# Performance work log

Hardware: AMD Instinct MI355X
Metric: run time of the kernel (lower is better)

## Reference

```python
import jax, jax.numpy as jnp
import numpy as np

GAMMA = 0.3   # LinearSpike surrogate slope
THR = 1.0     # default_threshold (all layers)
LEAK = 1.0
T = 20        # timesteps

# ---- surrogate-gradient spike functions ----
@jax.custom_vjp
def lin_spike(u):
    # forward: heaviside(u > 0); backward: gamma * max(1-|u|, 0)
    return (u > 0.0).astype(u.dtype)

def _ls_fwd(u):
    return lin_spike(u), u

def _ls_bwd(u, g):
    return (GAMMA * jnp.maximum(1.0 - jnp.abs(u), 0.0) * g,)

lin_spike.defvjp(_ls_fwd, _ls_bwd)

@jax.custom_vjp
def rect_spike(v):
    # threshold_rect: heaviside(v > 1); backward: 1[|v-1| < 0.5]
    return (v > 1.0).astype(v.dtype)

def _rs_fwd(v):
    return rect_spike(v), v

def _rs_bwd(v, g):
    return ((jnp.abs(v - 1.0) < 0.5).astype(g.dtype) * g,)

rect_spike.defvjp(_rs_fwd, _rs_bwd)


def conv3(x, w):
    # 3x3 conv, stride 1, SAME padding, no bias (matches bias=False Conv2d)
    return jax.lax.conv_general_dilated(
        x, w, (1, 1), 'SAME', dimension_numbers=('NCHW', 'OIHW', 'NCHW'))


def pool2(x):
    # AvgPool2d(kernel=2, stride=2)
    b, c, h, w = x.shape
    return x.reshape(b, c, h // 2, 2, w // 2, 2).mean(axis=(3, 5))


def setup_inputs() -> dict:
    key = jax.random.key(0)
    ks = jax.random.split(key, 7)
    B = 16
    x = jax.random.uniform(ks[0], (B, 3, 32, 32), jnp.float32)  # image in [0,1]

    def he(k, shape):  # _initialize_weights2 for conv: N(0, sqrt(2/(k*k*out_ch)))
        n = shape[0] * shape[2] * shape[3]
        return jax.random.normal(k, shape, jnp.float32) * np.float32(np.sqrt(2.0 / n))

    W1 = he(ks[1], (64, 3, 3, 3))
    W2 = he(ks[2], (128, 64, 3, 3))
    W3 = he(ks[3], (128, 128, 3, 3))
    # linears: N(0, 0.01), bias=False
    L1 = jax.random.normal(ks[4], (1024, 8192), jnp.float32) * 0.01
    L2 = jax.random.normal(ks[5], (1024, 1024), jnp.float32) * 0.01
    L3 = jax.random.normal(ks[6], (10, 1024), jnp.float32) * 0.01
    return {"x": x, "W1": W1, "W2": W2, "W3": W3, "L1": L1, "L2": L2, "L3": L3}


def reference(x, W1, W2, W3, L1, L2, L3):
    B = x.shape[0]
    dt = x.dtype
    z = lambda s: jnp.zeros(s, dt)
    carry = (z(x.shape), z(x.shape),           # encoder membrane v, last spike
             z((B, 64, 32, 32)),               # mem conv1
             z((B, 128, 16, 16)),              # mem conv2
             z((B, 128, 16, 16)),              # mem conv3
             z((B, 1024)), z((B, 1024)),       # mem fc1, fc2
             z((B, 10)))                       # output membrane (accumulator)

    def lif(mem, inp):
        # spike from current mem, soft reset by threshold, leaky integrate input
        out = lin_spike(mem / THR - 1.0)
        return LEAK * mem + inp - THR * out, out

    def step(c, _):
        v, s, m1, m2, m3, m4, m5, mo = c
        # if_encoder forward_2, soft reset: v = v + x*max_rate - spike
        v = v + x - s
        s = rect_spike(v)
        m1, o1 = lif(m1, conv3(s, W1))
        o1 = pool2(o1)                         # 32 -> 16
        m2, o2 = lif(m2, conv3(o1, W2))
        m3, o3 = lif(m3, conv3(o2, W3))
        f = pool2(o3).reshape(B, -1)           # 16 -> 8; flatten to 8192
        m4, o4 = lif(m4, f @ L1.T)
        m5, o5 = lif(m5, o4 @ L2.T)
        mo = mo + o5 @ L3.T                    # final linear accumulates membrane
        return (v, s, m1, m2, m3, m4, m5, mo), None

    carry, _ = jax.lax.scan(step, carry, None, length=T)
    return carry[-1]
```

## Files before the change

kernel.cpp:

```cpp
#include <hip/hip_runtime.h>

constexpr int BB   = 16;
constexpr int VS   = BB*3*32*32;
constexpr int M1N  = BB*64*32*32;
constexpr int O1PN = BB*64*18*20;
constexpr int M2N  = BB*128*16*16;
constexpr int O2PN = BB*128*18*20;
constexpr int M3N  = M2N;
constexpr int FBN  = BB*8192;
constexpr int M4N  = BB*1024;
constexpr int M5N  = BB*1024;

constexpr int off_v   = 0;
constexpr int off_s   = off_v   + 2*VS;
constexpr int off_m1  = off_s   + 2*VS;
constexpr int off_o1p = off_m1  + M1N;
constexpr int off_m2  = off_o1p + 2*O1PN;
constexpr int off_o2p = off_m2  + M2N;
constexpr int off_m3  = off_o2p + 2*O2PN;
constexpr int off_f   = off_m3  + M3N;
constexpr int off_m4  = off_f   + 2*FBN;
constexpr int off_o4  = off_m4  + M4N;
constexpr int off_m5  = off_o4  + 2*M4N;
constexpr int off_o5  = off_m5  + M5N;
constexpr int off_w1r = off_o5  + 2*M5N;
constexpr int W1RN = 64*3*12;
constexpr int off_w2r = off_w1r + W1RN;
constexpr int W2RN = 8*8*64*20;
constexpr int off_w3r = off_w2r + W2RN;
constexpr int W3RN = 8*8*128*20;
constexpr int TOTF = off_w3r + W3RN;

__device__ __forceinline__ float4 ld4(const float* p){ return *reinterpret_cast<const float4*>(p); }
__device__ __forceinline__ float2 ld2(const float* p){ return *reinterpret_cast<const float2*>(p); }
__device__ __forceinline__ float spk(float m){ return m > 1.0f ? 1.0f : 0.0f; }

__device__ __forceinline__ void gll16(const float* g, float* l) {
    __builtin_amdgcn_global_load_lds(
        (const __attribute__((address_space(1))) unsigned int*)g,
        (__attribute__((address_space(3))) unsigned int*)(unsigned int)(unsigned long long)l,
        16, 0, 0);
}

__global__ __launch_bounds__(256) void init_k(const float* __restrict__ W1,
                                              const float* __restrict__ W2,
                                              const float* __restrict__ W3,
                                              float* __restrict__ ws,
                                              float* __restrict__ out) {
    int i0 = blockIdx.x*256 + threadIdx.x;
    int stride = gridDim.x*256;
    for (int p = i0; p < TOTF; p += stride) {
        float val = 0.0f;
        if (p >= off_w1r) {
            if (p < off_w2r) {
                int l = p - off_w1r, q = l/12, r = l%12;
                int dx = r & 3, dy = r >> 2;
                val = (dx < 3) ? W1[q*9 + dy*3 + dx] : 0.0f;
            } else if (p < off_w3r) {
                int l = p - off_w2r;
                int cog = l / 10240, rem = l % 10240;
                int pr = rem / 1280, rem2 = rem % 1280;
                int ci = rem2 / 20, k = rem2 % 20;
                if (k < 18) {
                    int co = cog*16 + pr*2 + (k >= 9 ? 1 : 0);
                    int kk = k >= 9 ? k - 9 : k;
                    val = W2[(co*64 + ci)*9 + kk];
                }
            } else {
                int l = p - off_w3r;
                int cog = l / 20480, rem = l % 20480;
                int pr = rem / 2560, rem2 = rem % 2560;
                int ci = rem2 / 20, k = rem2 % 20;
                if (k < 18) {
                    int co = cog*16 + pr*2 + (k >= 9 ? 1 : 0);
                    int kk = k >= 9 ? k - 9 : k;
                    val = W3[(co*128 + ci)*9 + kk];
                }
            }
        }
        ws[p] = val;
    }
    if (i0 < 160) out[i0] = 0.0f;
}

#define CVW_LOAD(W, WQ) do {                                                   \
    _Pragma("unroll") for (int q_ = 0; q_ < 5; ++q_) W[q_] = ld4((WQ) + q_*4); } while(0)

#define CV4_FMA(Iu, Iv, W) do {                                                \
    float rv[4][6];                                                            \
    _Pragma("unroll") for (int r_ = 0; r_ < 4; ++r_) {                         \
        rv[r_][0]=Iu[r_].x; rv[r_][1]=Iu[r_].y; rv[r_][2]=Iu[r_].z;            \
        rv[r_][3]=Iu[r_].w; rv[r_][4]=Iv[r_].x; rv[r_][5]=Iv[r_].y; }          \
    float wd[2][9] = {{W[0].x,W[0].y,W[0].z,W[0].w,W[1].x,W[1].y,W[1].z,W[1].w,W[2].x}, \
                      {W[2].y,W[2].z,W[2].w,W[3].x,W[3].y,W[3].z,W[3].w,W[4].x,W[4].y}}; \
    _Pragma("unroll") for (int cc_ = 0; cc_ < 2; ++cc_)                        \
      _Pragma("unroll") for (int iy_ = 0; iy_ < 2; ++iy_)                      \
        _Pragma("unroll") for (int dy_ = 0; dy_ < 3; ++dy_)                    \
          _Pragma("unroll") for (int dx_ = 0; dx_ < 3; ++dx_) {                \
            float wv_ = wd[cc_][dy_*3+dx_];                                    \
            _Pragma("unroll") for (int p_ = 0; p_ < 4; ++p_)                   \
              acc[cc_][iy_][p_] += rv[iy_+dy_][p_+dx_]*wv_; } } while(0)

#define CVL_READ(Iu, Iv, P) do {                                               \
    _Pragma("unroll") for (int r_ = 0; r_ < 4; ++r_) {                         \
        Iu[r_] = ld4((P) + r_*28); Iv[r_] = ld2((P) + r_*28 + 4); } } while(0)

#define CV_STAGE(BUF, CH) do {                                                 \
    _Pragma("unroll") for (int k_ = 0; k_ < 4; ++k_) {                         \
        if (k_*256 + tid < 1008)                                               \
            gll16(gip + (CH)*2880 + ssrc[k_], sh + (BUF)*4032 + sdst[k_]);     \
    } } while(0)

__global__ __launch_bounds__(256) void step_k(const float* __restrict__ x,
                                              const float* __restrict__ L1,
                                              const float* __restrict__ L2,
                                              const float* __restrict__ L3,
                                              float* __restrict__ ws,
                                              float* __restrict__ out,
                                              int t) {
    const int rp = t & 1, wp = rp ^ 1;
    const int bid = blockIdx.x, tid = threadIdx.x;
    __shared__ __align__(16) float sh[8064];

    if (bid < 256) {
        const bool is3 = bid < 128;
        int bb = is3 ? bid : bid - 128;
        int b = bb >> 3, cog = bb & 7;
        int cl = tid >> 5, rest = tid & 31, rpair = rest >> 2, cg = rest & 3;
        int y0 = rpair*2, x0 = cg*4;
        int co = cog*16 + cl*2;
        const int NCI = is3 ? 128 : 64;
        const float* gip = is3 ? (ws + off_o2p + rp*O2PN + b*128*360)
                               : (ws + off_o1p + rp*O1PN + b*64*360);
        const float* wpt = is3 ? (ws + off_w3r + (cog*8 + cl)*128*20)
                               : (ws + off_w2r + (cog*8 + cl)*64*20);
        int ssrc[4], sdst[4];
        #pragma unroll
        for (int k = 0; k < 4; ++k) {
            int c = k*256 + tid;
            int u = c/126, rem = c - u*126, r = rem/7, j = rem - r*7;
            ssrc[k] = u*360 + (j < 5 ? 20*r + 4*j : 0);
            sdst[k] = c*4;
        }
        float acc[2][2][4] = {};
        float4 WA[5], WB[5];
        CVW_LOAD(WA, wpt);
        CVW_LOAD(WB, wpt + 20);
        CV_STAGE(0, 0);
        __syncthreads();
        const int NCH = NCI >> 3;
        #pragma unroll 1
        for (int ch = 0; ch < NCH; ++ch) {
            if (ch + 1 < NCH) CV_STAGE((ch+1)&1, ch+1);
            const float* lb = sh + (ch&1)*4032 + y0*28 + x0;
            #pragma unroll 1
            for (int u = 0; u < 8; u += 2) {
                int ci = ch*8 + u;
                {
                    float4 IAu[4]; float2 IAv[4];
                    CVL_READ(IAu, IAv, lb + u*504);
                    CV4_FMA(IAu, IAv, WA);
                    if (ci + 2 < NCI) CVW_LOAD(WA, wpt + (ci+2)*20);
                }
                {
                    float4 IBu[4]; float2 IBv[4];
                    CVL_READ(IBu, IBv, lb + u*504 + 504);
                    CV4_FMA(IBu, IBv, WB);
                    if (ci + 3 < NCI) CVW_LOAD(WB, wpt + (ci+3)*20);
                }
            }
            __syncthreads();
        }
        if (is3) {
            #pragma unroll
            for (int cc = 0; cc < 2; ++cc) {
                float sp[2][4];
                #pragma unroll
                for (int iy = 0; iy < 2; ++iy)
                    #pragma unroll
                    for (int p = 0; p < 4; ++p) {
                        int gm = off_m3 + ((b*128 + co + cc)*16 + y0 + iy)*16 + x0 + p;
                        float m = ws[gm], o = spk(m);
                        float mn = m + acc[cc][iy][p] - o;
                        ws[gm] = mn;
                        sp[iy][p] = spk(mn);
                    }
                int fbase = off_f + wp*FBN + b*8192 + (co + cc)*64 + (y0>>1)*8 + (x0>>1);
                ws[fbase+0] = (sp[0][0]+sp[0][1]+sp[1][0]+sp[1][1])*0.25f;
                ws[fbase+1] = (sp[0][2]+sp[0][3]+sp[1][2]+sp[1][3])*0.25f;
            }
        } else {
            #pragma unroll
            for (int cc = 0; cc < 2; ++cc) {
                #pragma unroll
                for (int iy = 0; iy < 2; ++iy) {
                    int mbase = off_m2 + ((b*128 + co + cc)*16 + y0 + iy)*16 + x0;
                    int obase = off_o2p + wp*O2PN + ((b*128 + co + cc)*18 + y0 + iy + 1)*20 + x0 + 1;
                    #pragma unroll
                    for (int p = 0; p < 4; ++p) {
                        float m = ws[mbase+p], o = spk(m);
                        float mn = m + acc[cc][iy][p] - o;
                        ws[mbase+p] = mn;
                        ws[obase+p] = spk(mn);
                    }
                }
            }
        }
    } else if (bid < 384) {
        int jb = bid - 256;
        int w = tid >> 6, l = tid & 63;
        const float* fp = ws + off_f + rp*FBN;
        const float* wb = L1 + (jb*8 + w*2)*8192;
        float acc[2][16] = {};
        float4 wA[2], wB[2];
        #pragma unroll
        for (int jj = 0; jj < 2; ++jj) {
            wA[jj] = ld4(wb + jj*8192 + l*4);
            wB[jj] = ld4(wb + jj*8192 + 256 + l*4);
        }
        for (int c = 0; c < 32; ++c) {
            const float* av = fp + c*256 + l*4;
            #pragma unroll
            for (int b = 0; b < 16; ++b) {
                float4 fv = ld4(av + b*8192);
                acc[0][b] += wA[0].x*fv.x + wA[0].y*fv.y + wA[0].z*fv.z + wA[0].w*fv.w;
                acc[1][b] += wA[1].x*fv.x + wA[1].y*fv.y + wA[1].z*fv.z + wA[1].w*fv.w;
            }
            wA[0] = wB[0]; wA[1] = wB[1];
            if (c < 30) {
                wB[0] = ld4(wb + (c+2)*256 + l*4);
                wB[1] = ld4(wb + 8192 + (c+2)*256 + l*4);
            }
        }
        #pragma unroll
        for (int jj = 0; jj < 2; ++jj)
            #pragma unroll
            for (int b = 0; b < 16; ++b) acc[jj][b] += __shfl_xor(acc[jj][b], 1);
        float* rg = sh + w*1056;
        if ((l & 1) == 0) {
            #pragma unroll
            for (int jj = 0; jj < 2; ++jj)
                #pragma unroll
                for (int b = 0; b < 16; ++b) rg[(l>>1)*33 + jj*16 + b] = acc[jj][b];
        }
        __syncthreads();
        if (tid < 128) {
            int w2 = tid >> 5, r = tid & 31, jj = r >> 4, b = r & 15;
            const float* rg2 = sh + w2*1056;
            float sum = 0.0f;
            #pragma unroll
            for (int l2 = 0; l2 < 32; ++l2) sum += rg2[l2*33 + r];
            int j = jb*8 + w2*2 + jj;
            int gi = off_m4 + b*1024 + j;
            float m = ws[gi], o = spk(m);
            float mn = m + sum - o;
            ws[gi] = mn;
            ws[off_o4 + wp*M4N + b*1024 + j] = spk(mn);
        }
    } else if (bid < 640) {
        int bb = bid - 384;
        int b = bb >> 4, tile = bb & 15;
        int ty = tile >> 2, tx = tile & 3;
        int y0 = ty*8, x0 = tx*8;
        const float* vin  = ws + off_v + rp*VS + b*3072;
        float*       vout = ws + off_v + wp*VS + b*3072;
        const float* sin_ = ws + off_s + rp*VS + b*3072;
        float*       sout = ws + off_s + wp*VS + b*3072;
        const float* xin  = x + b*3072;
        float* sl = sh;
        for (int idx = tid; idx < 300; idx += 256) {
            int ci = idx/100, r2 = idx%100, rr = r2/10, cc = r2%10;
            int yy = y0 - 1 + rr, xx = x0 - 1 + cc;
            float sv = 0.0f;
            if ((unsigned)yy < 32u && (unsigned)xx < 32u) {
                int g = ci*1024 + yy*32 + xx;
                float vn = vin[g] + xin[g] - sin_[g];
                sv = vn > 1.0f ? 1.0f : 0.0f;
                if (yy >= y0 && yy < y0+8 && xx >= x0 && xx < x0+8) { vout[g] = vn; sout[g] = sv; }
            }
            sl[(ci*10 + rr)*12 + cc] = sv;
        }
        __syncthreads();
        int tl = tid & 15, cog = tid >> 4;
        int py = (tl >> 2)*2, px = (tl & 3)*2;
        for (int cl = 0; cl < 4; ++cl) {
            int co = cog*4 + cl;
            const float* wtp = ws + off_w1r + co*36;
            float a00=0,a01=0,a10=0,a11=0;
            #pragma unroll
            for (int ci = 0; ci < 3; ++ci) {
                float4 w0 = ld4(wtp + ci*12), w1 = ld4(wtp + ci*12 + 4), w2 = ld4(wtp + ci*12 + 8);
                float wdl[3][3] = {{w0.x,w0.y,w0.z},{w1.x,w1.y,w1.z},{w2.x,w2.y,w2.z}};
                #pragma unroll
                for (int dy = 0; dy < 3; ++dy)
                    #pragma unroll
                    for (int dx = 0; dx < 3; ++dx) {
                        float wvv = wdl[dy][dx];
                        const float* rsl = sl + (ci*10 + py + dy)*12 + px + dx;
                        a00 += rsl[0]  * wvv; a01 += rsl[1]  * wvv;
                        a10 += rsl[12] * wvv; a11 += rsl[13] * wvv;
                    }
            }
            int gy = y0 + py, gx = x0 + px;
            float accs[2][2] = {{a00,a01},{a10,a11}};
            float pooled = 0.0f;
            #pragma unroll
            for (int iy = 0; iy < 2; ++iy)
                #pragma unroll
                for (int ix = 0; ix < 2; ++ix) {
                    int gm = off_m1 + ((b*64 + co)*32 + gy + iy)*32 + gx + ix;
                    float m = ws[gm], o = spk(m);
                    float mn = m + accs[iy][ix] - o;
                    ws[gm] = mn;
                    pooled += spk(mn);
                }
            ws[off_o1p + wp*O1PN + ((b*64 + co)*18 + (gy>>1) + 1)*20 + (gx>>1) + 1] = pooled*0.25f;
        }
    } else if (bid < 896) {
        int jb = bid - 640;
        int jg = tid >> 6, l = tid & 63;
        int j  = jb*4 + jg;
        const float* op = ws + off_o4 + rp*M4N;
        const float* wr = L2 + j*1024;
        float acc[16] = {};
        float4 wv[4];
        #pragma unroll
        for (int u = 0; u < 4; ++u) wv[u] = ld4(wr + u*256 + l*4);
        #pragma unroll
        for (int u = 0; u < 4; ++u) {
            int k = u*256 + l*4;
            #pragma unroll
            for (int b = 0; b < 16; ++b) {
                float4 fv = ld4(op + b*1024 + k);
                acc[b] += wv[u].x*fv.x + wv[u].y*fv.y + wv[u].z*fv.z + wv[u].w*fv.w;
            }
        }
        int r = jg*64 + l;
        #pragma unroll
        for (int b = 0; b < 16; ++b) sh[r*17 + b] = acc[b];
        __syncthreads();
        {
            int p = tid >> 2, q = tid & 3;
            float s2 = 0.0f;
            int rb2 = (p >> 4)*64 + q*16, col = p & 15;
            #pragma unroll
            for (int t2 = 0; t2 < 16; ++t2) s2 += sh[(rb2 + t2)*17 + col];
            sh[4352 + tid] = s2;
        }
        __syncthreads();
        if (tid < 64) {
            float sum = sh[4352 + tid*4] + sh[4352 + tid*4 + 1]
                      + sh[4352 + tid*4 + 2] + sh[4352 + tid*4 + 3];
            int jg2 = tid >> 4, b = tid & 15;
            int jj = jb*4 + jg2;
            int gi = off_m5 + b*1024 + jj;
            float m = ws[gi], o = spk(m);
            float mn = m + sum - o;
            ws[gi] = mn;
            ws[off_o5 + wp*M5N + b*1024 + jj] = spk(mn);
        }
    } else {
        if (tid < 160) {
            int b = tid/10, c = tid - b*10;
            const float* op = ws + off_o5 + rp*M5N + b*1024;
            const float* wr = L3 + c*1024;
            float sum = 0.0f;
            for (int k = 0; k < 1024; k += 4) {
                float4 a = ld4(op + k), wvv = ld4(wr + k);
                sum += a.x*wvv.x + a.y*wvv.y + a.z*wvv.z + a.w*wvv.w;
            }
            out[b*10 + c] += sum;
        }
    }
}

extern "C" void kernel_launch(void* const* d_in, const int* in_sizes, int n_in,
                              void* d_out, int out_size, void* d_ws, size_t ws_size,
                              hipStream_t stream) {
    const float* x  = (const float*)d_in[0];
    const float* W1 = (const float*)d_in[1];
    const float* W2 = (const float*)d_in[2];
    const float* W3 = (const float*)d_in[3];
    const float* L1 = (const float*)d_in[4];
    const float* L2 = (const float*)d_in[5];
    const float* L3 = (const float*)d_in[6];
    float* out = (float*)d_out;
    float* ws  = (float*)d_ws;

    init_k<<<1024, 256, 0, stream>>>(W1, W2, W3, ws, out);
    for (int t = 0; t < 20; ++t)
        step_k<<<897, 256, 0, stream>>>(x, L1, L2, L3, ws, out, t);
}
```

Measured before the change: 1.298 ms.

## Split conv2/conv3 blocks by row half to double block count

```diff
diff --git a/kernel.cpp b/kernel.cpp
--- a/kernel.cpp
+++ b/kernel.cpp
@@ -86,29 +86,28 @@
 #define CVW_LOAD(W, WQ) do {                                                   \
     _Pragma("unroll") for (int q_ = 0; q_ < 5; ++q_) W[q_] = ld4((WQ) + q_*4); } while(0)
 
-#define CV4_FMA(Iu, Iv, W) do {                                                \
-    float rv[4][6];                                                            \
-    _Pragma("unroll") for (int r_ = 0; r_ < 4; ++r_) {                         \
+#define CV1_FMA(Iu, Iv, W) do {                                                \
+    float rv[3][6];                                                            \
+    _Pragma("unroll") for (int r_ = 0; r_ < 3; ++r_) {                         \
         rv[r_][0]=Iu[r_].x; rv[r_][1]=Iu[r_].y; rv[r_][2]=Iu[r_].z;            \
         rv[r_][3]=Iu[r_].w; rv[r_][4]=Iv[r_].x; rv[r_][5]=Iv[r_].y; }          \
     float wd[2][9] = {{W[0].x,W[0].y,W[0].z,W[0].w,W[1].x,W[1].y,W[1].z,W[1].w,W[2].x}, \
                       {W[2].y,W[2].z,W[2].w,W[3].x,W[3].y,W[3].z,W[3].w,W[4].x,W[4].y}}; \
     _Pragma("unroll") for (int cc_ = 0; cc_ < 2; ++cc_)                        \
-      _Pragma("unroll") for (int iy_ = 0; iy_ < 2; ++iy_)                      \
-        _Pragma("unroll") for (int dy_ = 0; dy_ < 3; ++dy_)                    \
-          _Pragma("unroll") for (int dx_ = 0; dx_ < 3; ++dx_) {                \
+      _Pragma("unroll") for (int dy_ = 0; dy_ < 3; ++dy_)                      \
+        _Pragma("unroll") for (int dx_ = 0; dx_ < 3; ++dx_) {                  \
             float wv_ = wd[cc_][dy_*3+dx_];                                    \
             _Pragma("unroll") for (int p_ = 0; p_ < 4; ++p_)                   \
-              acc[cc_][iy_][p_] += rv[iy_+dy_][p_+dx_]*wv_; } } while(0)
+              acc[cc_][p_] += rv[dy_][p_+dx_]*wv_; } } while(0)
 
 #define CVL_READ(Iu, Iv, P) do {                                               \
-    _Pragma("unroll") for (int r_ = 0; r_ < 4; ++r_) {                         \
+    _Pragma("unroll") for (int r_ = 0; r_ < 3; ++r_) {                         \
         Iu[r_] = ld4((P) + r_*28); Iv[r_] = ld2((P) + r_*28 + 4); } } while(0)
 
 #define CV_STAGE(BUF, CH) do {                                                 \
-    _Pragma("unroll") for (int k_ = 0; k_ < 4; ++k_) {                         \
-        if (k_*256 + tid < 1008)                                               \
-            gll16(gip + (CH)*2880 + ssrc[k_], sh + (BUF)*4032 + sdst[k_]);     \
+    _Pragma("unroll") for (int k_ = 0; k_ < 3; ++k_) {                         \
+        if (k_*256 + tid < 560)                                                \
+            gll16(gip + (CH)*2880 + ssrc[k_], sh + (BUF)*2240 + sdst[k_]);     \
     } } while(0)
 
 __global__ __launch_bounds__(256) void step_k(const float* __restrict__ x,
@@ -120,29 +119,30 @@
                                               int t) {
     const int rp = t & 1, wp = rp ^ 1;
     const int bid = blockIdx.x, tid = threadIdx.x;
-    __shared__ __align__(16) float sh[8064];
-
-    if (bid < 256) {
-        const bool is3 = bid < 128;
-        int bb = is3 ? bid : bid - 128;
-        int b = bb >> 3, cog = bb & 7;
-        int cl = tid >> 5, rest = tid & 31, rpair = rest >> 2, cg = rest & 3;
-        int y0 = rpair*2, x0 = cg*4;
+    __shared__ __align__(16) float sh[4608];
+
+    if (bid < 512) {
+        const bool is3 = bid < 256;
+        int bb = is3 ? bid : bid - 256;
+        int b = bb >> 4, sub = bb & 15, cog = sub >> 1, yh = sub & 1;
+        int cl = tid >> 5, rest = tid & 31, y = rest >> 2, xg = rest & 3;
+        int x0 = xg*4;
         int co = cog*16 + cl*2;
+        int Y = yh*8 + y;
         const int NCI = is3 ? 128 : 64;
         const float* gip = is3 ? (ws + off_o2p + rp*O2PN + b*128*360)
                                : (ws + off_o1p + rp*O1PN + b*64*360);
         const float* wpt = is3 ? (ws + off_w3r + (cog*8 + cl)*128*20)
                                : (ws + off_w2r + (cog*8 + cl)*64*20);
-        int ssrc[4], sdst[4];
-        #pragma unroll
-        for (int k = 0; k < 4; ++k) {
+        int ssrc[3], sdst[3];
+        #pragma unroll
+        for (int k = 0; k < 3; ++k) {
             int c = k*256 + tid;
-            int u = c/126, rem = c - u*126, r = rem/7, j = rem - r*7;
-            ssrc[k] = u*360 + (j < 5 ? 20*r + 4*j : 0);
+            int u = c/70, rem = c - u*70, r = rem/7, j = rem - r*7;
+            ssrc[k] = u*360 + (yh*8 + r)*20 + (j < 5 ? j*4 : 0);
             sdst[k] = c*4;
         }
-        float acc[2][2][4] = {};
+        float acc[2][4] = {};
         float4 WA[5], WB[5];
         CVW_LOAD(WA, wpt);
         CVW_LOAD(WB, wpt + 20);
@@ -152,20 +152,20 @@
         #pragma unroll 1
         for (int ch = 0; ch < NCH; ++ch) {
             if (ch + 1 < NCH) CV_STAGE((ch+1)&1, ch+1);
-            const float* lb = sh + (ch&1)*4032 + y0*28 + x0;
+            const float* lb = sh + (ch&1)*2240 + y*28 + x0;
             #pragma unroll 1
             for (int u = 0; u < 8; u += 2) {
                 int ci = ch*8 + u;
                 {
-                    float4 IAu[4]; float2 IAv[4];
-                    CVL_READ(IAu, IAv, lb + u*504);
-                    CV4_FMA(IAu, IAv, WA);
+                    float4 IAu[3]; float2 IAv[3];
+                    CVL_READ(IAu, IAv, lb + u*280);
+                    CV1_FMA(IAu, IAv, WA);
                     if (ci + 2 < NCI) CVW_LOAD(WA, wpt + (ci+2)*20);
                 }
                 {
-                    float4 IBu[4]; float2 IBv[4];
-                    CVL_READ(IBu, IBv, lb + u*504 + 504);
-                    CV4_FMA(IBu, IBv, WB);
+                    float4 IBu[3]; float2 IBv[3];
+                    CVL_READ(IBu, IBv, lb + u*280 + 280);
+                    CV1_FMA(IBu, IBv, WB);
                     if (ci + 3 < NCI) CVW_LOAD(WB, wpt + (ci+3)*20);
                 }
             }
@@ -174,40 +174,39 @@
         if (is3) {
             #pragma unroll
             for (int cc = 0; cc < 2; ++cc) {
-                float sp[2][4];
-                #pragma unroll
-                for (int iy = 0; iy < 2; ++iy)
-                    #pragma unroll
-                    for (int p = 0; p < 4; ++p) {
-                        int gm = off_m3 + ((b*128 + co + cc)*16 + y0 + iy)*16 + x0 + p;
-                        float m = ws[gm], o = spk(m);
-                        float mn = m + acc[cc][iy][p] - o;
-                        ws[gm] = mn;
-                        sp[iy][p] = spk(mn);
-                    }
-                int fbase = off_f + wp*FBN + b*8192 + (co + cc)*64 + (y0>>1)*8 + (x0>>1);
-                ws[fbase+0] = (sp[0][0]+sp[0][1]+sp[1][0]+sp[1][1])*0.25f;
-                ws[fbase+1] = (sp[0][2]+sp[0][3]+sp[1][2]+sp[1][3])*0.25f;
+                float sp[4];
+                #pragma unroll
+                for (int p = 0; p < 4; ++p) {
+                    int gm = off_m3 + ((b*128 + co + cc)*16 + Y)*16 + x0 + p;
+                    float m = ws[gm], o = spk(m);
+                    float mn = m + acc[cc][p] - o;
+                    ws[gm] = mn;
+                    sp[p] = spk(mn);
+                }
+                float pl = sp[0] + sp[1], ph = sp[2] + sp[3];
+                float ql = __shfl_xor(pl, 4), qh = __shfl_xor(ph, 4);
+                if ((y & 1) == 0) {
+                    int fbase = off_f + wp*FBN + b*8192 + (co + cc)*64 + (Y>>1)*8 + (x0>>1);
+                    ws[fbase+0] = (pl + ql)*0.25f;
+                    ws[fbase+1] = (ph + qh)*0.25f;
+                }
             }
         } else {
             #pragma unroll
             for (int cc = 0; cc < 2; ++cc) {
-                #pragma unroll
-                for (int iy = 0; iy < 2; ++iy) {
-                    int mbase = off_m2 + ((b*128 + co + cc)*16 + y0 + iy)*16 + x0;
-                    int obase = off_o2p + wp*O2PN + ((b*128 + co + cc)*18 + y0 + iy + 1)*20 + x0 + 1;
-                    #pragma unroll
-                    for (int p = 0; p < 4; ++p) {
-                        float m = ws[mbase+p], o = spk(m);
-                        float mn = m + acc[cc][iy][p] - o;
-                        ws[mbase+p] = mn;
-                        ws[obase+p] = spk(mn);
-                    }
-                }
-            }
-        }
-    } else if (bid < 384) {
-        int jb = bid - 256;
+                int mbase = off_m2 + ((b*128 + co + cc)*16 + Y)*16 + x0;
+                int obase = off_o2p + wp*O2PN + ((b*128 + co + cc)*18 + Y + 1)*20 + x0 + 1;
+                #pragma unroll
+                for (int p = 0; p < 4; ++p) {
+                    float m = ws[mbase+p], o = spk(m);
+                    float mn = m + acc[cc][p] - o;
+                    ws[mbase+p] = mn;
+                    ws[obase+p] = spk(mn);
+                }
+            }
+        }
+    } else if (bid < 640) {
+        int jb = bid - 512;
         int w = tid >> 6, l = tid & 63;
         const float* fp = ws + off_f + rp*FBN;
         const float* wb = L1 + (jb*8 + w*2)*8192;
@@ -257,8 +256,8 @@
             ws[gi] = mn;
             ws[off_o4 + wp*M4N + b*1024 + j] = spk(mn);
         }
-    } else if (bid < 640) {
-        int bb = bid - 384;
+    } else if (bid < 896) {
+        int bb = bid - 640;
         int b = bb >> 4, tile = bb & 15;
         int ty = tile >> 2, tx = tile & 3;
         int y0 = ty*8, x0 = tx*8;
@@ -316,8 +315,8 @@
                 }
             ws[off_o1p + wp*O1PN + ((b*64 + co)*18 + (gy>>1) + 1)*20 + (gx>>1) + 1] = pooled*0.25f;
         }
-    } else if (bid < 896) {
-        int jb = bid - 640;
+    } else if (bid < 1152) {
+        int jb = bid - 896;
         int jg = tid >> 6, l = tid & 63;
         int j  = jb*4 + jg;
         const float* op = ws + off_o4 + rp*M4N;
@@ -389,5 +388,5 @@
 
     init_k<<<1024, 256, 0, stream>>>(W1, W2, W3, ws, out);
     for (int t = 0; t < 20; ++t)
-        step_k<<<897, 256, 0, stream>>>(x, L1, L2, L3, ws, out, t);
+        step_k<<<1153, 256, 0, stream>>>(x, L1, L2, L3, ws, out, t);
 }
```

Measured after the change: 1.543 ms. +18.9%, slower.

## Split conv2/conv3 input channels across two half-blocks and pack other roles pairwise

Applied to the files above, without the earlier changes.

```diff
diff --git a/kernel.cpp b/kernel.cpp
--- a/kernel.cpp
+++ b/kernel.cpp
@@ -107,11 +107,11 @@
 
 #define CV_STAGE(BUF, CH) do {                                                 \
     _Pragma("unroll") for (int k_ = 0; k_ < 4; ++k_) {                         \
-        if (k_*256 + tid < 1008)                                               \
-            gll16(gip + (CH)*2880 + ssrc[k_], sh + (BUF)*4032 + sdst[k_]);     \
+        if (k_*256 + ltid < 1008)                                              \
+            gll16(gip + (CH)*2880 + ssrc[k_], shb + (BUF)*4032 + sdst[k_]);    \
     } } while(0)
 
-__global__ __launch_bounds__(256) void step_k(const float* __restrict__ x,
+__global__ __launch_bounds__(512) void step_k(const float* __restrict__ x,
                                               const float* __restrict__ L1,
                                               const float* __restrict__ L2,
                                               const float* __restrict__ L3,
@@ -120,95 +120,117 @@
                                               int t) {
     const int rp = t & 1, wp = rp ^ 1;
     const int bid = blockIdx.x, tid = threadIdx.x;
-    __shared__ __align__(16) float sh[8064];
+    const int h2 = tid >> 8, ltid = tid & 255;
+    __shared__ __align__(16) float sh[16128];
 
     if (bid < 256) {
         const bool is3 = bid < 128;
         int bb = is3 ? bid : bid - 128;
         int b = bb >> 3, cog = bb & 7;
-        int cl = tid >> 5, rest = tid & 31, rpair = rest >> 2, cg = rest & 3;
+        int cl = ltid >> 5, rest = ltid & 31, rpair = rest >> 2, cg = rest & 3;
         int y0 = rpair*2, x0 = cg*4;
         int co = cog*16 + cl*2;
-        const int NCI = is3 ? 128 : 64;
-        const float* gip = is3 ? (ws + off_o2p + rp*O2PN + b*128*360)
-                               : (ws + off_o1p + rp*O1PN + b*64*360);
+        const int NCI = is3 ? 128 : 64, HALF = NCI >> 1, NCHH = HALF >> 3;
+        const int ciBase = h2*HALF, ciHi = ciBase + HALF;
+        const float* gip = (is3 ? (ws + off_o2p + rp*O2PN + b*128*360)
+                                : (ws + off_o1p + rp*O1PN + b*64*360)) + ciBase*360;
         const float* wpt = is3 ? (ws + off_w3r + (cog*8 + cl)*128*20)
                                : (ws + off_w2r + (cog*8 + cl)*64*20);
+        float* shb = sh + h2*8064;
         int ssrc[4], sdst[4];
         #pragma unroll
         for (int k = 0; k < 4; ++k) {
-            int c = k*256 + tid;
+            int c = k*256 + ltid;
             int u = c/126, rem = c - u*126, r = rem/7, j = rem - r*7;
             ssrc[k] = u*360 + (j < 5 ? 20*r + 4*j : 0);
             sdst[k] = c*4;
         }
         float acc[2][2][4] = {};
         float4 WA[5], WB[5];
-        CVW_LOAD(WA, wpt);
-        CVW_LOAD(WB, wpt + 20);
+        CVW_LOAD(WA, wpt + ciBase*20);
+        CVW_LOAD(WB, wpt + ciBase*20 + 20);
         CV_STAGE(0, 0);
         __syncthreads();
-        const int NCH = NCI >> 3;
         #pragma unroll 1
-        for (int ch = 0; ch < NCH; ++ch) {
-            if (ch + 1 < NCH) CV_STAGE((ch+1)&1, ch+1);
-            const float* lb = sh + (ch&1)*4032 + y0*28 + x0;
+        for (int ch = 0; ch < NCHH; ++ch) {
+            if (ch + 1 < NCHH) CV_STAGE((ch+1)&1, ch+1);
+            const float* lb = shb + (ch&1)*4032 + y0*28 + x0;
             #pragma unroll 1
             for (int u = 0; u < 8; u += 2) {
-                int ci = ch*8 + u;
+                int ci = ciBase + ch*8 + u;
                 {
                     float4 IAu[4]; float2 IAv[4];
                     CVL_READ(IAu, IAv, lb + u*504);
                     CV4_FMA(IAu, IAv, WA);
-                    if (ci + 2 < NCI) CVW_LOAD(WA, wpt + (ci+2)*20);
+                    if (ci + 2 < ciHi) CVW_LOAD(WA, wpt + (ci+2)*20);
                 }
                 {
                     float4 IBu[4]; float2 IBv[4];
                     CVL_READ(IBu, IBv, lb + u*504 + 504);
                     CV4_FMA(IBu, IBv, WB);
-                    if (ci + 3 < NCI) CVW_LOAD(WB, wpt + (ci+3)*20);
+                    if (ci + 3 < ciHi) CVW_LOAD(WB, wpt + (ci+3)*20);
                 }
             }
             __syncthreads();
         }
-        if (is3) {
-            #pragma unroll
-            for (int cc = 0; cc < 2; ++cc) {
-                float sp[2][4];
+        if (h2 == 1) {
+            float* rg = sh + ltid*17;
+            #pragma unroll
+            for (int cc = 0; cc < 2; ++cc)
                 #pragma unroll
                 for (int iy = 0; iy < 2; ++iy)
                     #pragma unroll
-                    for (int p = 0; p < 4; ++p) {
-                        int gm = off_m3 + ((b*128 + co + cc)*16 + y0 + iy)*16 + x0 + p;
-                        float m = ws[gm], o = spk(m);
-                        float mn = m + acc[cc][iy][p] - o;
-                        ws[gm] = mn;
-                        sp[iy][p] = spk(mn);
+                    for (int p = 0; p < 4; ++p) rg[cc*8 + iy*4 + p] = acc[cc][iy][p];
+        }
+        __syncthreads();
+        if (h2 == 0) {
+            const float* rg = sh + ltid*17;
+            #pragma unroll
+            for (int cc = 0; cc < 2; ++cc)
+                #pragma unroll
+                for (int iy = 0; iy < 2; ++iy)
+                    #pragma unroll
+                    for (int p = 0; p < 4; ++p) acc[cc][iy][p] += rg[cc*8 + iy*4 + p];
+            if (is3) {
+                #pragma unroll
+                for (int cc = 0; cc < 2; ++cc) {
+                    float sp[2][4];
+                    #pragma unroll
+                    for (int iy = 0; iy < 2; ++iy)
+                        #pragma unroll
+                        for (int p = 0; p < 4; ++p) {
+                            int gm = off_m3 + ((b*128 + co + cc)*16 + y0 + iy)*16 + x0 + p;
+                            float m = ws[gm], o = spk(m);
+                            float mn = m + acc[cc][iy][p] - o;
+                            ws[gm] = mn;
+                            sp[iy][p] = spk(mn);
+                        }
+                    int fbase = off_f + wp*FBN + b*8192 + (co + cc)*64 + (y0>>1)*8 + (x0>>1);
+                    ws[fbase+0] = (sp[0][0]+sp[0][1]+sp[1][0]+sp[1][1])*0.25f;
+                    ws[fbase+1] = (sp[0][2]+sp[0][3]+sp[1][2]+sp[1][3])*0.25f;
+                }
+            } else {
+                #pragma unroll
+                for (int cc = 0; cc < 2; ++cc) {
+                    #pragma unroll
+                    for (int iy = 0; iy < 2; ++iy) {
+                        int mbase = off_m2 + ((b*128 + co + cc)*16 + y0 + iy)*16 + x0;
+                        int obase = off_o2p + wp*O2PN + ((b*128 + co + cc)*18 + y0 + iy + 1)*20 + x0 + 1;
+                        #pragma unroll
+                        for (int p = 0; p < 4; ++p) {
+                            float m = ws[mbase+p], o = spk(m);
+                            float mn = m + acc[cc][iy][p] - o;
+                            ws[mbase+p] = mn;
+                            ws[obase+p] = spk(mn);
+                        }
                     }
-                int fbase = off_f + wp*FBN + b*8192 + (co + cc)*64 + (y0>>1)*8 + (x0>>1);
-                ws[fbase+0] = (sp[0][0]+sp[0][1]+sp[1][0]+sp[1][1])*0.25f;
-                ws[fbase+1] = (sp[0][2]+sp[0][3]+sp[1][2]+sp[1][3])*0.25f;
-            }
-        } else {
-            #pragma unroll
-            for (int cc = 0; cc < 2; ++cc) {
-                #pragma unroll
-                for (int iy = 0; iy < 2; ++iy) {
-                    int mbase = off_m2 + ((b*128 + co + cc)*16 + y0 + iy)*16 + x0;
-                    int obase = off_o2p + wp*O2PN + ((b*128 + co + cc)*18 + y0 + iy + 1)*20 + x0 + 1;
-                    #pragma unroll
-                    for (int p = 0; p < 4; ++p) {
-                        float m = ws[mbase+p], o = spk(m);
-                        float mn = m + acc[cc][iy][p] - o;
-                        ws[mbase+p] = mn;
-                        ws[obase+p] = spk(mn);
-                    }
-                }
-            }
-        }
-    } else if (bid < 384) {
-        int jb = bid - 256;
-        int w = tid >> 6, l = tid & 63;
+                }
+            }
+        }
+    } else if (bid < 320) {
+        int jb = (bid - 256)*2 + h2;
+        int w = ltid >> 6, l = ltid & 63;
+        float* shh = sh + h2*4224;
         const float* fp = ws + off_f + rp*FBN;
         const float* wb = L1 + (jb*8 + w*2)*8192;
         float acc[2][16] = {};
@@ -236,7 +258,7 @@
         for (int jj = 0; jj < 2; ++jj)
             #pragma unroll
             for (int b = 0; b < 16; ++b) acc[jj][b] += __shfl_xor(acc[jj][b], 1);
-        float* rg = sh + w*1056;
+        float* rg = shh + w*1056;
         if ((l & 1) == 0) {
             #pragma unroll
             for (int jj = 0; jj < 2; ++jj)
@@ -244,9 +266,9 @@
                 for (int b = 0; b < 16; ++b) rg[(l>>1)*33 + jj*16 + b] = acc[jj][b];
         }
         __syncthreads();
-        if (tid < 128) {
-            int w2 = tid >> 5, r = tid & 31, jj = r >> 4, b = r & 15;
-            const float* rg2 = sh + w2*1056;
+        if (ltid < 128) {
+            int w2 = ltid >> 5, r = ltid & 31, jj = r >> 4, b = r & 15;
+            const float* rg2 = shh + w2*1056;
             float sum = 0.0f;
             #pragma unroll
             for (int l2 = 0; l2 < 32; ++l2) sum += rg2[l2*33 + r];
@@ -257,9 +279,9 @@
             ws[gi] = mn;
             ws[off_o4 + wp*M4N + b*1024 + j] = spk(mn);
         }
-    } else if (bid < 640) {
-        int bb = bid - 384;
-        int b = bb >> 4, tile = bb & 15;
+    } else if (bid < 448) {
+        int bb2 = (bid - 320)*2 + h2;
+        int b = bb2 >> 4, tile = bb2 & 15;
         int ty = tile >> 2, tx = tile & 3;
         int y0 = ty*8, x0 = tx*8;
         const float* vin  = ws + off_v + rp*VS + b*3072;
@@ -267,8 +289,8 @@
         const float* sin_ = ws + off_s + rp*VS + b*3072;
         float*       sout = ws + off_s + wp*VS + b*3072;
         const float* xin  = x + b*3072;
-        float* sl = sh;
-        for (int idx = tid; idx < 300; idx += 256) {
+        float* sl = sh + h2*384;
+        for (int idx = ltid; idx < 300; idx += 256) {
             int ci = idx/100, r2 = idx%100, rr = r2/10, cc = r2%10;
             int yy = y0 - 1 + rr, xx = x0 - 1 + cc;
             float sv = 0.0f;
@@ -281,7 +303,7 @@
             sl[(ci*10 + rr)*12 + cc] = sv;
         }
         __syncthreads();
-        int tl = tid & 15, cog = tid >> 4;
+        int tl = ltid & 15, cog = ltid >> 4;
         int py = (tl >> 2)*2, px = (tl & 3)*2;
         for (int cl = 0; cl < 4; ++cl) {
             int co = cog*4 + cl;
@@ -316,10 +338,11 @@
                 }
             ws[off_o1p + wp*O1PN + ((b*64 + co)*18 + (gy>>1) + 1)*20 + (gx>>1) + 1] = pooled*0.25f;
         }
-    } else if (bid < 896) {
-        int jb = bid - 640;
-        int jg = tid >> 6, l = tid & 63;
+    } else if (bid < 576) {
+        int jb = (bid - 448)*2 + h2;
+        int jg = ltid >> 6, l = ltid & 63;
         int j  = jb*4 + jg;
+        float* shh = sh + h2*4608;
         const float* op = ws + off_o4 + rp*M4N;
         const float* wr = L2 + j*1024;
         float acc[16] = {};
@@ -337,21 +360,21 @@
         }
         int r = jg*64 + l;
         #pragma unroll
-        for (int b = 0; b < 16; ++b) sh[r*17 + b] = acc[b];
+        for (int b = 0; b < 16; ++b) shh[r*17 + b] = acc[b];
         __syncthreads();
         {
-            int p = tid >> 2, q = tid & 3;
+            int p = ltid >> 2, q = ltid & 3;
             float s2 = 0.0f;
             int rb2 = (p >> 4)*64 + q*16, col = p & 15;
             #pragma unroll
-            for (int t2 = 0; t2 < 16; ++t2) s2 += sh[(rb2 + t2)*17 + col];
-            sh[4352 + tid] = s2;
-        }
-        __syncthreads();
-        if (tid < 64) {
-            float sum = sh[4352 + tid*4] + sh[4352 + tid*4 + 1]
-                      + sh[4352 + tid*4 + 2] + sh[4352 + tid*4 + 3];
-            int jg2 = tid >> 4, b = tid & 15;
+            for (int t2 = 0; t2 < 16; ++t2) s2 += shh[(rb2 + t2)*17 + col];
+            shh[4352 + ltid] = s2;
+        }
+        __syncthreads();
+        if (ltid < 64) {
+            float sum = shh[4352 + ltid*4] + shh[4352 + ltid*4 + 1]
+                      + shh[4352 + ltid*4 + 2] + shh[4352 + ltid*4 + 3];
+            int jg2 = ltid >> 4, b = ltid & 15;
             int jj = jb*4 + jg2;
             int gi = off_m5 + b*1024 + jj;
             float m = ws[gi], o = spk(m);
@@ -389,5 +412,5 @@
 
     init_k<<<1024, 256, 0, stream>>>(W1, W2, W3, ws, out);
     for (int t = 0; t < 20; ++t)
-        step_k<<<897, 256, 0, stream>>>(x, L1, L2, L3, ws, out, t);
+        step_k<<<577, 512, 0, stream>>>(x, L1, L2, L3, ws, out, t);
 }
```

New measurement: 1.503 ms. +15.8%, slower.
